# Kernel tuning notes

Hardware: AMD Instinct MI355X
Metric: run time of the kernel (lower is better)

Reference implementation:

```python
import jax, jax.numpy as jnp
import numpy as np

B, T, M, P = 256, 256, 256, 256  # batch, timesteps, encoder hidden m, decoder hidden p


def setup_inputs() -> dict:
    key = jax.random.key(0)
    ks = jax.random.split(key, 12)
    def n(k, shape, s=0.05):
        return jax.random.normal(k, shape, dtype=jnp.float32) * s
    return {
        "data": n(ks[0], (B, T - 1, 1), 1.0),          # decoder inputs y_1..y_{T-1}
        "encoder_h": n(ks[1], (B, T, M), 1.0),          # encoder hidden states
        "h0": jnp.zeros((B, P), jnp.float32),
        "s0": jnp.zeros((B, P), jnp.float32),
        # dense: Dense(1) on concat([x, context]) -> input dim 1+M
        "Wd": n(ks[2], (1 + M, 1)), "bd": jnp.zeros((1,), jnp.float32),
        # decoder LSTM (Keras gate order i,f,c,o): kernel (1,4P), recurrent (P,4P)
        "Wk": n(ks[3], (1, 4 * P)), "Wr": n(ks[4], (P, 4 * P)), "bl": jnp.zeros((4 * P,), jnp.float32),
        # temporal attention: W: 2P->M, U: M->M, v: M->1
        "Ww": n(ks[5], (2 * P, M)), "bw": jnp.zeros((M,), jnp.float32),
        "Wu": n(ks[6], (M, M)), "bu": jnp.zeros((M,), jnp.float32),
        "Wv": n(ks[7], (M, 1)), "bv": jnp.zeros((1,), jnp.float32),
        # output head: densevb: P+M -> 1, denseWb: 1 -> P
        "Wvb": n(ks[8], (P + M, 1)), "bvb": jnp.zeros((1,), jnp.float32),
        "Wwb": n(ks[9], (1, P)), "bwb": jnp.zeros((P,), jnp.float32),
    }


def reference(data, encoder_h, h0, s0, Wd, bd, Wk, Wr, bl, Ww, bw,
              Wu, bu, Wv, bv, Wvb, bvb, Wwb, bwb):
    # Hoist U(encoder_h) out of the time loop: it does not depend on t (same math).
    Ue = encoder_h @ Wu + bu                      # (B, T, M)
    xs = jnp.transpose(data, (1, 0, 2))           # (T-1, B, 1) for scan
    ctx0 = jnp.zeros((data.shape[0], Ue.shape[-1]), data.dtype)  # initial context (B, M)

    def step(carry, x_t):
        h, s, ctx = carry                          # (B,P), (B,P), (B,M)
        # y_tilde = Dense(1)(concat([x_t, context]))
        y = jnp.concatenate([x_t, ctx], axis=-1) @ Wd + bd        # (B, 1)
        # single-step Keras LSTM cell, gates i, f, c, o
        z = y @ Wk + h @ Wr + bl                   # (B, 4P)
        i, f, g, o = jnp.split(z, 4, axis=-1)
        s_new = jax.nn.sigmoid(f) * s + jax.nn.sigmoid(i) * jnp.tanh(g)
        h_new = jax.nn.sigmoid(o) * jnp.tanh(s_new)
        # temporal attention: l = v(tanh(W(repeat(concat[h,s])) + U(encoder_h)))
        dsc = jnp.concatenate([h_new, s_new], axis=-1) @ Ww + bw  # (B, M)
        l = jnp.tanh(dsc[:, None, :] + Ue) @ Wv + bv              # (B, T, 1)
        beta = jax.nn.softmax(l, axis=1)                          # softmax over time axis
        # context = beta^T @ encoder_h -> (B, M)
        ctx_new = jnp.sum(beta * encoder_h, axis=1)
        return (h_new, s_new, ctx_new), None

    (h, s, ctx), _ = jax.lax.scan(step, (h0, s0, ctx0), xs)
    cat = jnp.concatenate([h, ctx], axis=-1)[:, None, :]          # (B, 1, P+M)
    # denseWb(densevb(concatenated)): (P+M)->1 then 1->P, as in the source
    return (cat @ Wvb + bvb) @ Wwb + bwb                          # (B, 1, P)
```

## Files before the change

kernel.cpp:

```cpp
#include <hip/hip_runtime.h>
#include <hip/hip_bf16.h>

#define B 256
#define T 256
#define M 256
#define P 256
#define TSTEPS 255
#define NT 1024
#define RG 6
#define RA 8

typedef unsigned int uint;
typedef _Float16 hf2 __attribute__((ext_vector_type(2)));

__device__ __forceinline__ float fast_tanh(float x) {
    float e = exp2f(x * 2.885390082f);
    return 1.f - 2.f * __builtin_amdgcn_rcpf(e + 1.f);
}
__device__ __forceinline__ float fast_sigmoid(float x) {
    float e = exp2f(-x * 1.442695041f);
    return __builtin_amdgcn_rcpf(1.f + e);
}

#if defined(__has_builtin)
#if __has_builtin(__builtin_amdgcn_fdot2)
#define HAVE_FDOT2 1
#endif
#endif

__device__ __forceinline__ float dot2(uint a, uint b, float c) {
#ifdef HAVE_FDOT2
    return __builtin_amdgcn_fdot2(__builtin_bit_cast(hf2, a),
                                  __builtin_bit_cast(hf2, b), c, false);
#else
    hf2 x = __builtin_bit_cast(hf2, a), y = __builtin_bit_cast(hf2, b);
    return c + (float)x.x * (float)y.x + (float)x.y * (float)y.y;
#endif
}

__device__ __forceinline__ uint pk16(float a, float b) {
    return __builtin_bit_cast(uint, __builtin_amdgcn_cvt_pkrtz(a, b));
}

__global__ __launch_bounds__(256) void ue_gemm(
    const float* __restrict__ enc, const float* __restrict__ Wu,
    const float* __restrict__ bu, _Float16* __restrict__ Ue16)
{
    __shared__ float At[32][256];
    const int r0 = blockIdx.x * 32;
    const int tid = threadIdx.x;

    #pragma unroll 4
    for (int i = 0; i < 32; ++i)
        At[i][tid] = enc[(size_t)(r0 + i) * 256 + tid];
    __syncthreads();

    float acc[32];
    #pragma unroll
    for (int r = 0; r < 32; ++r) acc[r] = 0.f;

    for (int k = 0; k < 256; k += 4) {
        float w0 = Wu[(size_t)(k + 0) * 256 + tid];
        float w1 = Wu[(size_t)(k + 1) * 256 + tid];
        float w2 = Wu[(size_t)(k + 2) * 256 + tid];
        float w3 = Wu[(size_t)(k + 3) * 256 + tid];
        #pragma unroll
        for (int r = 0; r < 32; ++r) {
            float4 a4 = *(const float4*)&At[r][k];
            acc[r] += a4.x * w0 + a4.y * w1 + a4.z * w2 + a4.w * w3;
        }
    }
    float bub = bu[tid];
    #pragma unroll 4
    for (int r = 0; r < 32; ++r)
        Ue16[(size_t)(r0 + r) * 256 + tid] =
            (_Float16)exp2f(1.442695041f * (acc[r] + bub));
}

__global__ __launch_bounds__(256) void wr_cvt(
    const float* __restrict__ Wr, uint4* __restrict__ Wsz)
{
    int i = blockIdx.x * 256 + threadIdx.x;
    int kc = i >> 10, c = i & 1023;
    const float* s = Wr + (size_t)kc * 8 * 1024 + c;
    uint4 o;
    o.x = pk16(s[0 * 1024], s[1 * 1024]);
    o.y = pk16(s[2 * 1024], s[3 * 1024]);
    o.z = pk16(s[4 * 1024], s[5 * 1024]);
    o.w = pk16(s[6 * 1024], s[7 * 1024]);
    Wsz[i] = o;
}

__global__ __launch_bounds__(256) void ww_cvt(
    const float* __restrict__ Ww, uint4* __restrict__ Wwsz)
{
    int i = blockIdx.x * 256 + threadIdx.x;
    int kk = i >> 8, m = i & 255;
    const float* s = Ww + (size_t)kk * 8 * 256 + m;
    uint4 o;
    o.x = pk16(s[0 * 256], s[1 * 256]);
    o.y = pk16(s[2 * 256], s[3 * 256]);
    o.z = pk16(s[4 * 256], s[5 * 256]);
    o.w = pk16(s[6 * 256], s[7 * 256]);
    Wwsz[i] = o;
}

__global__ __launch_bounds__(NT, 4) void decoder_scan(
    const float* __restrict__ data,
    const float* __restrict__ h0,  const float* __restrict__ s0,
    const float* __restrict__ Wd,  const float* __restrict__ bd,
    const float* __restrict__ Wk,  const float* __restrict__ bl,
    const float* __restrict__ bw,
    const float* __restrict__ Wv,  const float* __restrict__ bv,
    const float* __restrict__ Wvb, const float* __restrict__ bvb,
    const float* __restrict__ Wwb, const float* __restrict__ bwb,
    const float* __restrict__ enc,
    const _Float16* __restrict__ Ue16g,
    const uint4* __restrict__ Wsz, const uint4* __restrict__ Wwsz,
    float* __restrict__ out)
{
    const int b    = blockIdx.x;
    const int tid  = threadIdx.x;
    const int lane = tid & 63;
    const int wave = tid >> 6;

    __shared__ _Float16 ue_lds[T * M];
    __shared__ float h_lds[P], s_lds[P];
    __shared__ __align__(16) uint hs2[128 + 4 + 128];
    __shared__ float z_lds[4 * 257];
    __shared__ __align__(16) uint  edup[2][132];
    __shared__ __align__(16) float wv2dup[2][264];
    __shared__ float el_lds[T];
    __shared__ float g_lds[T];
    __shared__ float ctx_lds[M];
    __shared__ __align__(16) float sred[8], yred[8];
    __shared__ float ya[4];
    __shared__ float data_lds[TSTEPS + 1];
    __shared__ int aflag;

    uint* h2_lds = hs2;
    uint* s2_lds = hs2 + 132;

    {
        const uint4* src = (const uint4*)(Ue16g + (size_t)b * T * M);
        uint4* dst = (uint4*)ue_lds;
        #pragma unroll
        for (int i = 0; i < 8; ++i) {
            int g = tid + i * NT;
            uint4 v = src[g];
            int r = g >> 5, lin = g & 31;
            int phys = (lin & 16) | ((lin ^ (2 * r + (lin >> 4))) & 15);
            dst[(r << 5) + phys] = v;
        }
    }
    if (tid == 0) aflag = 0;
    if (tid < 256) {
        float hv = h0[b * 256 + tid], sv = s0[b * 256 + tid];
        h_lds[tid] = hv; s_lds[tid] = sv; ctx_lds[tid] = 0.f;
        float w2 = 2.f * Wv[tid];
        wv2dup[0][tid] = w2; wv2dup[1][tid] = w2;
        float hv1 = __shfl_down(hv, 1, 64);
        float sv1 = __shfl_down(sv, 1, 64);
        if (!(tid & 1)) {
            h2_lds[tid >> 1] = pk16(hv, hv1);
            s2_lds[tid >> 1] = pk16(sv, sv1);
        }
    }
    if (tid < 8) { sred[tid] = 1.f; yred[tid] = 0.f; }
    if (tid < TSTEPS) data_lds[tid] = data[b * TSTEPS + tid];

    const float Wd0 = Wd[0], bd0 = bd[0];
    const float* encB = enc + (size_t)b * T * M;

    {
        float w0 = Wd[1 + lane * 4], w1 = Wd[2 + lane * 4];
        float w2 = Wd[3 + lane * 4], w3 = Wd[4 + lane * 4];
        for (int i = 0; i < 16; ++i) {
            int tp = wave * 16 + i;
            float4 e4 = *(const float4*)&encB[(size_t)tp * 256 + lane * 4];
            float p = e4.x * w0 + e4.y * w1 + e4.z * w2 + e4.w * w3;
            #pragma unroll
            for (int mm = 32; mm >= 1; mm >>= 1) p += __shfl_xor(p, mm, 64);
            if (lane == 0) g_lds[tp] = p;
        }
    }
    __syncthreads();

    const uint4* h2u4 = (const uint4*)h2_lds;
    const uint4* s2u4 = (const uint4*)s2_lds;

    {
        const uint4* wc = Wsz + tid;
        float acc = 0.f;
        #pragma unroll 4
        for (int kc = 0; kc < 32; ++kc) {
            uint4 w = wc[kc << 10];
            uint4 h = h2u4[kc];
            acc = dot2(w.x, h.x, acc); acc = dot2(w.y, h.y, acc);
            acc = dot2(w.z, h.z, acc); acc = dot2(w.w, h.w, acc);
        }
        z_lds[(tid >> 8) * 257 + (tid & 255)] = acc;
    }
    __syncthreads();

    if (wave < 8) {
        const int gate = tid & 3, uu0 = tid >> 2, uu1 = uu0 + 128;
        const int cz0 = gate * 257 + uu0, cz1 = gate * 257 + uu1;
        const float wk0 = Wk[gate * 256 + uu0], bl0 = bl[gate * 256 + uu0];
        const float wk1 = Wk[gate * 256 + uu1], bl1 = bl[gate * 256 + uu1];
        const int zr = tid >> 8, zc = tid & 255;
        const uint4* wcA = Wsz + tid;
        const uint4* wcB = Wsz + tid + 512;
        uint4 rA[RG], rB[RG];
        #pragma unroll
        for (int kc = 0; kc < RG; ++kc) { rA[kc] = wcA[kc << 10]; rB[kc] = wcB[kc << 10]; }

        for (int t = 0; t < TSTEPS; ++t) {
            uint4 pA0 = wcA[(RG + 0) << 10], pB0 = wcB[(RG + 0) << 10];
            uint4 pA1 = wcA[(RG + 1) << 10], pB1 = wcB[(RG + 1) << 10];

            {
                float4 sa = *(const float4*)&sred[0], sb = *(const float4*)&sred[4];
                float4 yaa = *(const float4*)&yred[0], yab = *(const float4*)&yred[4];
                float S = sa.x + sa.y + sa.z + sa.w + sb.x + sb.y + sb.z + sb.w;
                float Y = yaa.x + yaa.y + yaa.z + yaa.w + yab.x + yab.y + yab.z + yab.w;
                float ys = Y * __builtin_amdgcn_rcpf(S) + data_lds[t] * Wd0 + bd0;
                float zc0 = z_lds[cz0] + ys * wk0 + bl0;
                float zc1 = z_lds[cz1] + ys * wk1 + bl1;
                float nl0 = (gate == 2) ? fast_tanh(zc0) : fast_sigmoid(zc0);
                float nl1 = (gate == 2) ? fast_tanh(zc1) : fast_sigmoid(zc1);
                float a1 = __shfl_xor(nl0, 1, 64);
                float a2 = __shfl_xor(nl0, 2, 64);
                float a3 = __shfl_xor(nl0, 3, 64);
                float b1 = __shfl_xor(nl1, 1, 64);
                float b2 = __shfl_xor(nl1, 2, 64);
                float b3 = __shfl_xor(nl1, 3, 64);
                float hn0 = 0.f, sv0 = 0.f, hn1 = 0.f, sv1 = 0.f;
                if (gate == 0) {
                    sv0 = a1 * s_lds[uu0] + nl0 * a2;
                    hn0 = a3 * fast_tanh(sv0);
                    sv1 = b1 * s_lds[uu1] + nl1 * b2;
                    hn1 = b3 * fast_tanh(sv1);
                    s_lds[uu0] = sv0; h_lds[uu0] = hn0;
                    s_lds[uu1] = sv1; h_lds[uu1] = hn1;
                }
                float hd0 = __shfl_down(hn0, 4, 64), sd0 = __shfl_down(sv0, 4, 64);
                float hd1 = __shfl_down(hn1, 4, 64), sd1 = __shfl_down(sv1, 4, 64);
                if ((tid & 7) == 0) {
                    h2_lds[uu0 >> 1] = pk16(hn0, hd0); s2_lds[uu0 >> 1] = pk16(sv0, sd0);
                    h2_lds[uu1 >> 1] = pk16(hn1, hd1); s2_lds[uu1 >> 1] = pk16(sv1, sd1);
                }
            }
            __syncthreads();
            float a0 = 0.f, a1 = 0.f;
            #pragma unroll
            for (int kc = 0; kc < RG; ++kc) {
                uint4 h = h2u4[kc];
                a0 = dot2(rA[kc].x, h.x, a0); a0 = dot2(rA[kc].y, h.y, a0);
                a0 = dot2(rA[kc].z, h.z, a0); a0 = dot2(rA[kc].w, h.w, a0);
                a1 = dot2(rB[kc].x, h.x, a1); a1 = dot2(rB[kc].y, h.y, a1);
                a1 = dot2(rB[kc].z, h.z, a1); a1 = dot2(rB[kc].w, h.w, a1);
            }
            {
                uint4 h = h2u4[RG];
                a0 = dot2(pA0.x, h.x, a0); a0 = dot2(pA0.y, h.y, a0);
                a0 = dot2(pA0.z, h.z, a0); a0 = dot2(pA0.w, h.w, a0);
                a1 = dot2(pB0.x, h.x, a1); a1 = dot2(pB0.y, h.y, a1);
                a1 = dot2(pB0.z, h.z, a1); a1 = dot2(pB0.w, h.w, a1);
            }
            {
                uint4 h = h2u4[RG + 1];
                a0 = dot2(pA1.x, h.x, a0); a0 = dot2(pA1.y, h.y, a0);
                a0 = dot2(pA1.z, h.z, a0); a0 = dot2(pA1.w, h.w, a0);
                a1 = dot2(pB1.x, h.x, a1); a1 = dot2(pB1.y, h.y, a1);
                a1 = dot2(pB1.z, h.z, a1); a1 = dot2(pB1.w, h.w, a1);
            }
            #pragma unroll 4
            for (int kc = RG + 2; kc < 32; ++kc) {
                uint4 wA = wcA[kc << 10], wB = wcB[kc << 10];
                uint4 h = h2u4[kc];
                a0 = dot2(wA.x, h.x, a0); a0 = dot2(wA.y, h.y, a0);
                a0 = dot2(wA.z, h.z, a0); a0 = dot2(wA.w, h.w, a0);
                a1 = dot2(wB.x, h.x, a1); a1 = dot2(wB.y, h.y, a1);
                a1 = dot2(wB.z, h.z, a1); a1 = dot2(wB.w, h.w, a1);
            }
            z_lds[zr * 257 + zc] = a0;
            z_lds[(2 + zr) * 257 + zc] = a1;
            __syncthreads();
        }
    } else {
        const int aw  = wave - 8;
        const int aid = tid - 512;
        const int dm  = aid >> 1;
        const int dkh = aid & 1;
        const int ekey = aid & 15;
        const float bwm = bw[dm];
        const uint4* wwp  = Wwsz + (dkh << 13) + dm;
        const uint4* uecT = (const uint4*)ue_lds + (aid << 4);
        const uint4*  edT = (const uint4*)(&edup[dkh][0]) + (dkh << 4);
        const float4* wvT = (const float4*)(&wv2dup[dkh][0]) + (dkh << 5);
        const uint4* cat4 = dkh ? s2u4 : h2u4;
        uint4 rW[RA];
        #pragma unroll
        for (int i = 0; i < RA; ++i) rW[i] = wwp[i << 8];

        for (int t = 0; t < TSTEPS; ++t) {
            uint4 e0 = wwp[(RA + 0) << 8], e1 = wwp[(RA + 1) << 8];
            uint4 e2 = wwp[(RA + 2) << 8], e3 = wwp[(RA + 3) << 8];
            __syncthreads();
            float a = 0.f;
            #pragma unroll
            for (int i = 0; i < RA; ++i) {
                uint4 c = cat4[i];
                a = dot2(rW[i].x, c.x, a); a = dot2(rW[i].y, c.y, a);
                a = dot2(rW[i].z, c.z, a); a = dot2(rW[i].w, c.w, a);
            }
            {
                uint4 c = cat4[RA + 0];
                a = dot2(e0.x, c.x, a); a = dot2(e0.y, c.y, a);
                a = dot2(e0.z, c.z, a); a = dot2(e0.w, c.w, a);
                c = cat4[RA + 1];
                a = dot2(e1.x, c.x, a); a = dot2(e1.y, c.y, a);
                a = dot2(e1.z, c.z, a); a = dot2(e1.w, c.w, a);
                c = cat4[RA + 2];
                a = dot2(e2.x, c.x, a); a = dot2(e2.y, c.y, a);
                a = dot2(e2.z, c.z, a); a = dot2(e2.w, c.w, a);
                c = cat4[RA + 3];
                a = dot2(e3.x, c.x, a); a = dot2(e3.y, c.y, a);
                a = dot2(e3.z, c.z, a); a = dot2(e3.w, c.w, a);
            }
            #pragma unroll 4
            for (int i = RA + 4; i < 32; ++i) {
                uint4 w = wwp[i << 8];
                uint4 c = cat4[i];
                a = dot2(w.x, c.x, a); a = dot2(w.y, c.y, a);
                a = dot2(w.z, c.z, a); a = dot2(w.w, c.w, a);
            }
            a += __shfl_xor(a, 1, 64);
            float ed = exp2f(1.442695041f * (a + bwm));
            float ed2 = __shfl_xor(ed, 2, 64);
            if ((aid & 3) == 0) {
                uint u = pk16(ed, ed2);
                edup[0][dm >> 1] = u;
                edup[1][dm >> 1] = u;
            }
            __threadfence_block();
            if (lane == 0) atomicAdd(&aflag, 1);
            const int tgt = 8 * (t + 1);
            while (*(volatile int*)&aflag < tgt) {}
            __threadfence_block();

            __builtin_amdgcn_s_setprio(1);
            float pl = 0.f;
            #pragma unroll 4
            for (int jj = 0; jj < 16; ++jj) {
                uint4 u = uecT[jj ^ ekey];
                uint4 d = edT[jj];
                float4 wA = wvT[jj * 2], wB = wvT[jj * 2 + 1];
                hf2 p0 = __builtin_bit_cast(hf2, u.x) * __builtin_bit_cast(hf2, d.x);
                hf2 p1 = __builtin_bit_cast(hf2, u.y) * __builtin_bit_cast(hf2, d.y);
                hf2 p2 = __builtin_bit_cast(hf2, u.z) * __builtin_bit_cast(hf2, d.z);
                hf2 p3 = __builtin_bit_cast(hf2, u.w) * __builtin_bit_cast(hf2, d.w);
                p0 = p0 * p0; p1 = p1 * p1; p2 = p2 * p2; p3 = p3 * p3;
                {
                    float a0 = fminf((float)p0.x, 1e18f) + 1.f;
                    float a1 = fminf((float)p0.y, 1e18f) + 1.f;
                    float qq = __builtin_amdgcn_rcpf(a0 * a1);
                    pl = fmaf(wA.x, a1 * qq, pl);
                    pl = fmaf(wA.y, a0 * qq, pl);
                }
                {
                    float a0 = fminf((float)p1.x, 1e18f) + 1.f;
                    float a1 = fminf((float)p1.y, 1e18f) + 1.f;
                    float qq = __builtin_amdgcn_rcpf(a0 * a1);
                    pl = fmaf(wA.z, a1 * qq, pl);
                    pl = fmaf(wA.w, a0 * qq, pl);
                }
                {
                    float a0 = fminf((float)p2.x, 1e18f) + 1.f;
                    float a1 = fminf((float)p2.y, 1e18f) + 1.f;
                    float qq = __builtin_amdgcn_rcpf(a0 * a1);
                    pl = fmaf(wB.x, a1 * qq, pl);
                    pl = fmaf(wB.y, a0 * qq, pl);
                }
                {
                    float a0 = fminf((float)p3.x, 1e18f) + 1.f;
                    float a1 = fminf((float)p3.y, 1e18f) + 1.f;
                    float qq = __builtin_amdgcn_rcpf(a0 * a1);
                    pl = fmaf(wB.z, a1 * qq, pl);
                    pl = fmaf(wB.w, a0 * qq, pl);
                }
            }
            pl += __shfl_xor(pl, 1, 64);
            float ev = exp2f(-1.442695041f * pl);
            if (!dkh) el_lds[dm] = ev;
            float yg = ev * g_lds[dm];
            #pragma unroll
            for (int mm = 2; mm <= 32; mm <<= 1) {
                ev += __shfl_xor(ev, mm, 64);
                yg += __shfl_xor(yg, mm, 64);
            }
            if (lane == 0) { sred[aw] = ev; yred[aw] = yg; }
            __builtin_amdgcn_s_setprio(0);
            __syncthreads();
        }
    }

    {
        float S;
        {
            float4 sa = *(const float4*)&sred[0], sb = *(const float4*)&sred[4];
            S = sa.x + sa.y + sa.z + sa.w + sb.x + sb.y + sb.z + sb.w;
        }
        float a0 = 0.f, a1 = 0.f, a2 = 0.f, a3 = 0.f;
        for (int i = 0; i < 16; ++i) {
            int tp = wave * 16 + i;
            float w = el_lds[tp];
            float4 e4 = *(const float4*)&encB[(size_t)tp * 256 + lane * 4];
            a0 += w * e4.x; a1 += w * e4.y; a2 += w * e4.z; a3 += w * e4.w;
        }
        atomicAdd(&ctx_lds[lane * 4 + 0], a0);
        atomicAdd(&ctx_lds[lane * 4 + 1], a1);
        atomicAdd(&ctx_lds[lane * 4 + 2], a2);
        atomicAdd(&ctx_lds[lane * 4 + 3], a3);
        __syncthreads();

        float qp = 0.f;
        if (tid < 256) {
            float ctx = ctx_lds[tid] * __builtin_amdgcn_rcpf(S);
            qp = h_lds[tid] * Wvb[tid] + ctx * Wvb[256 + tid];
        }
        if (wave < 4) {
            #pragma unroll
            for (int mm = 32; mm >= 1; mm >>= 1) qp += __shfl_xor(qp, mm, 64);
            if (lane == 0) ya[wave] = qp;
        }
        __syncthreads();
        if (tid < 256) {
            float qv = ya[0] + ya[1] + ya[2] + ya[3] + bvb[0];
            out[b * 256 + tid] = qv * Wwb[tid] + bwb[tid];
        }
    }
}

extern "C" void kernel_launch(void* const* d_in, const int* in_sizes, int n_in,
                              void* d_out, int out_size, void* d_ws, size_t ws_size,
                              hipStream_t stream) {
    const float* data = (const float*)d_in[0];
    const float* enc  = (const float*)d_in[1];
    const float* h0   = (const float*)d_in[2];
    const float* s0   = (const float*)d_in[3];
    const float* Wd   = (const float*)d_in[4];
    const float* bd   = (const float*)d_in[5];
    const float* Wk   = (const float*)d_in[6];
    const float* Wr   = (const float*)d_in[7];
    const float* bl   = (const float*)d_in[8];
    const float* Ww   = (const float*)d_in[9];
    const float* bw   = (const float*)d_in[10];
    const float* Wu   = (const float*)d_in[11];
    const float* bu   = (const float*)d_in[12];
    const float* Wv   = (const float*)d_in[13];
    const float* bv   = (const float*)d_in[14];
    const float* Wvb  = (const float*)d_in[15];
    const float* bvb  = (const float*)d_in[16];
    const float* Wwb  = (const float*)d_in[17];
    const float* bwb  = (const float*)d_in[18];

    _Float16* Ue16 = (_Float16*)d_ws;
    uint4* Wsz  = (uint4*)((char*)d_ws + (32ull << 20));
    uint4* Wwsz = (uint4*)((char*)d_ws + (32ull << 20) + (512ull << 10));
    float* out = (float*)d_out;

    hipLaunchKernelGGL(ue_gemm, dim3((B * T) / 32), dim3(256), 0, stream,
                       enc, Wu, bu, Ue16);
    hipLaunchKernelGGL(wr_cvt, dim3(128), dim3(256), 0, stream, Wr, Wsz);
    hipLaunchKernelGGL(ww_cvt, dim3(64), dim3(256), 0, stream, Ww, Wwsz);
    hipLaunchKernelGGL(decoder_scan, dim3(B), dim3(NT), 0, stream,
                       data, h0, s0, Wd, bd, Wk, bl, bw,
                       Wv, bv, Wvb, bvb, Wwb, bwb,
                       enc, Ue16, Wsz, Wwsz, out);
}
```

Before: 2.820 ms.

## Keep Ue slice in registers and stage half of Ww in LDS

Each attention thread now holds its 16 uint4 of the fp16 Ue tile in registers instead of reading it from a swizzled LDS copy. The freed 128KB of LDS now holds half of the Ww weights, so the attention dot product reads those from LDS rather than global memory or L2. The gate path drops its prefetch registers, pins the resident weight registers with an asm barrier, and the spin-wait gains s_sleep. The cost is much higher register pressure in the attention waves, which may cause spills or lower occupancy, and s_sleep may add latency to the barrier.

```diff
diff --git a/kernel.cpp b/kernel.cpp
--- a/kernel.cpp
+++ b/kernel.cpp
@@ -8,10 +8,11 @@
 #define TSTEPS 255
 #define NT 1024
 #define RG 6
-#define RA 8
 
 typedef unsigned int uint;
 typedef _Float16 hf2 __attribute__((ext_vector_type(2)));
+
+#define KEEP4(v) asm volatile("" : "+v"((v).x), "+v"((v).y), "+v"((v).z), "+v"((v).w))
 
 __device__ __forceinline__ float fast_tanh(float x) {
     float e = exp2f(x * 2.885390082f);
@@ -124,7 +125,7 @@
     const int lane = tid & 63;
     const int wave = tid >> 6;
 
-    __shared__ _Float16 ue_lds[T * M];
+    __shared__ __align__(16) uint4 ww_lds[2 * 16 * 256];
     __shared__ float h_lds[P], s_lds[P];
     __shared__ __align__(16) uint hs2[128 + 4 + 128];
     __shared__ float z_lds[4 * 257];
@@ -142,15 +143,11 @@
     uint* s2_lds = hs2 + 132;
 
     {
-        const uint4* src = (const uint4*)(Ue16g + (size_t)b * T * M);
-        uint4* dst = (uint4*)ue_lds;
         #pragma unroll
-        for (int i = 0; i < 8; ++i) {
-            int g = tid + i * NT;
-            uint4 v = src[g];
-            int r = g >> 5, lin = g & 31;
-            int phys = (lin & 16) | ((lin ^ (2 * r + (lin >> 4))) & 15);
-            dst[(r << 5) + phys] = v;
+        for (int k = 0; k < 8; ++k) {
+            int l = tid + k * NT;
+            int m = l & 255, i = (l >> 8) & 15, dk = l >> 12;
+            ww_lds[l] = Wwsz[((dk * 32 + i) << 8) + m];
         }
     }
     if (tid == 0) aflag = 0;
@@ -213,12 +210,12 @@
         const uint4* wcB = Wsz + tid + 512;
         uint4 rA[RG], rB[RG];
         #pragma unroll
-        for (int kc = 0; kc < RG; ++kc) { rA[kc] = wcA[kc << 10]; rB[kc] = wcB[kc << 10]; }
+        for (int kc = 0; kc < RG; ++kc) {
+            rA[kc] = wcA[kc << 10]; rB[kc] = wcB[kc << 10];
+            KEEP4(rA[kc]); KEEP4(rB[kc]);
+        }
 
         for (int t = 0; t < TSTEPS; ++t) {
-            uint4 pA0 = wcA[(RG + 0) << 10], pB0 = wcB[(RG + 0) << 10];
-            uint4 pA1 = wcA[(RG + 1) << 10], pB1 = wcB[(RG + 1) << 10];
-
             {
                 float4 sa = *(const float4*)&sred[0], sb = *(const float4*)&sred[4];
                 float4 yaa = *(const float4*)&yred[0], yab = *(const float4*)&yred[4];
@@ -252,6 +249,7 @@
                 }
             }
             __syncthreads();
+
             float a0 = 0.f, a1 = 0.f;
             #pragma unroll
             for (int kc = 0; kc < RG; ++kc) {
@@ -261,22 +259,8 @@
                 a1 = dot2(rB[kc].x, h.x, a1); a1 = dot2(rB[kc].y, h.y, a1);
                 a1 = dot2(rB[kc].z, h.z, a1); a1 = dot2(rB[kc].w, h.w, a1);
             }
-            {
-                uint4 h = h2u4[RG];
-                a0 = dot2(pA0.x, h.x, a0); a0 = dot2(pA0.y, h.y, a0);
-                a0 = dot2(pA0.z, h.z, a0); a0 = dot2(pA0.w, h.w, a0);
-                a1 = dot2(pB0.x, h.x, a1); a1 = dot2(pB0.y, h.y, a1);
-                a1 = dot2(pB0.z, h.z, a1); a1 = dot2(pB0.w, h.w, a1);
-            }
-            {
-                uint4 h = h2u4[RG + 1];
-                a0 = dot2(pA1.x, h.x, a0); a0 = dot2(pA1.y, h.y, a0);
-                a0 = dot2(pA1.z, h.z, a0); a0 = dot2(pA1.w, h.w, a0);
-                a1 = dot2(pB1.x, h.x, a1); a1 = dot2(pB1.y, h.y, a1);
-                a1 = dot2(pB1.z, h.z, a1); a1 = dot2(pB1.w, h.w, a1);
-            }
             #pragma unroll 4
-            for (int kc = RG + 2; kc < 32; ++kc) {
+            for (int kc = RG; kc < 32; ++kc) {
                 uint4 wA = wcA[kc << 10], wB = wcB[kc << 10];
                 uint4 h = h2u4[kc];
                 a0 = dot2(wA.x, h.x, a0); a0 = dot2(wA.y, h.y, a0);
@@ -293,44 +277,32 @@
         const int aid = tid - 512;
         const int dm  = aid >> 1;
         const int dkh = aid & 1;
-        const int ekey = aid & 15;
         const float bwm = bw[dm];
         const uint4* wwp  = Wwsz + (dkh << 13) + dm;
-        const uint4* uecT = (const uint4*)ue_lds + (aid << 4);
+        const uint4* wwl  = ww_lds + (dkh << 12) + dm;
         const uint4*  edT = (const uint4*)(&edup[dkh][0]) + (dkh << 4);
         const float4* wvT = (const float4*)(&wv2dup[dkh][0]) + (dkh << 5);
         const uint4* cat4 = dkh ? s2u4 : h2u4;
-        uint4 rW[RA];
-        #pragma unroll
-        for (int i = 0; i < RA; ++i) rW[i] = wwp[i << 8];
+
+        uint4 eu[16];
+        {
+            const uint4* eusrc = (const uint4*)(Ue16g + (size_t)b * T * M) + (aid << 4);
+            #pragma unroll
+            for (int i = 0; i < 16; ++i) { eu[i] = eusrc[i]; KEEP4(eu[i]); }
+        }
 
         for (int t = 0; t < TSTEPS; ++t) {
-            uint4 e0 = wwp[(RA + 0) << 8], e1 = wwp[(RA + 1) << 8];
-            uint4 e2 = wwp[(RA + 2) << 8], e3 = wwp[(RA + 3) << 8];
             __syncthreads();
             float a = 0.f;
-            #pragma unroll
-            for (int i = 0; i < RA; ++i) {
+            #pragma unroll 4
+            for (int i = 0; i < 16; ++i) {
+                uint4 w = wwl[i << 8];
                 uint4 c = cat4[i];
-                a = dot2(rW[i].x, c.x, a); a = dot2(rW[i].y, c.y, a);
-                a = dot2(rW[i].z, c.z, a); a = dot2(rW[i].w, c.w, a);
-            }
-            {
-                uint4 c = cat4[RA + 0];
-                a = dot2(e0.x, c.x, a); a = dot2(e0.y, c.y, a);
-                a = dot2(e0.z, c.z, a); a = dot2(e0.w, c.w, a);
-                c = cat4[RA + 1];
-                a = dot2(e1.x, c.x, a); a = dot2(e1.y, c.y, a);
-                a = dot2(e1.z, c.z, a); a = dot2(e1.w, c.w, a);
-                c = cat4[RA + 2];
-                a = dot2(e2.x, c.x, a); a = dot2(e2.y, c.y, a);
-                a = dot2(e2.z, c.z, a); a = dot2(e2.w, c.w, a);
-                c = cat4[RA + 3];
-                a = dot2(e3.x, c.x, a); a = dot2(e3.y, c.y, a);
-                a = dot2(e3.z, c.z, a); a = dot2(e3.w, c.w, a);
+                a = dot2(w.x, c.x, a); a = dot2(w.y, c.y, a);
+                a = dot2(w.z, c.z, a); a = dot2(w.w, c.w, a);
             }
             #pragma unroll 4
-            for (int i = RA + 4; i < 32; ++i) {
+            for (int i = 16; i < 32; ++i) {
                 uint4 w = wwp[i << 8];
                 uint4 c = cat4[i];
                 a = dot2(w.x, c.x, a); a = dot2(w.y, c.y, a);
@@ -347,14 +319,14 @@
             __threadfence_block();
             if (lane == 0) atomicAdd(&aflag, 1);
             const int tgt = 8 * (t + 1);
-            while (*(volatile int*)&aflag < tgt) {}
+            while (*(volatile int*)&aflag < tgt) __builtin_amdgcn_s_sleep(1);
             __threadfence_block();
 
             __builtin_amdgcn_s_setprio(1);
             float pl = 0.f;
-            #pragma unroll 4
+            #pragma unroll
             for (int jj = 0; jj < 16; ++jj) {
-                uint4 u = uecT[jj ^ ekey];
+                uint4 u = eu[jj];
                 uint4 d = edT[jj];
                 float4 wA = wvT[jj * 2], wB = wvT[jj * 2 + 1];
                 hf2 p0 = __builtin_bit_cast(hf2, u.x) * __builtin_bit_cast(hf2, d.x);
```

Measured after the change: 2.644 ms. 6.2% less time.
